# Performance work log

Hardware: AMD Instinct MI355X
Metric: run time of the kernel (lower is better)

## Reference

```python
import jax, jax.numpy as jnp
import numpy as np


def _average(x, w, W):
    """layers.Average forward: weighted mean over batch of Linear(x) (bias=False).
    x: [N, d_in], w: [N, 1], W: [d_out, d_in] -> [1, d_out]"""
    h = x @ W.T                                    # [N, d_out]
    return jnp.sum(h * w, axis=0, keepdims=True) / jnp.sum(w)


def setup_inputs() -> dict:
    key = jax.random.key(0)
    k1, k2, k3, k4 = jax.random.split(key, 4)
    N, n_in, n_middle = 1_000_000, 32, 128
    x = jax.random.normal(k1, (N, n_in), dtype=jnp.float32)
    w = jax.random.uniform(k2, (N, 1), dtype=jnp.float32)
    # Linear weights (Kaiming-ish scale), bias=False per __init__ default
    W_in = jax.random.normal(k3, (n_middle, n_in), dtype=jnp.float32) / np.float32(np.sqrt(n_in))
    W_out = jax.random.normal(k4, (n_in, n_middle), dtype=jnp.float32) / np.float32(np.sqrt(n_middle))
    return {"x": x, "w": w, "W_in": W_in, "W_out": W_out}


def reference(x, w, W_in, W_out):
    # x_ = activation(avg_in(x, w))
    h = jax.nn.relu(_average(x, w, W_in))          # [1, n_middle]
    # x_ = avg_out(x_, w); residual add (broadcast over batch)
    x_ = _average(h, w, W_out)                     # [1, n_in]
    return x + x_                                  # [N, n_in]
```

## Files before the change

### kernel.cpp

```cpp
#include <hip/hip_runtime.h>

#define BS 256
#define NB1 2048
#define NB3 2048

typedef float vfloat4 __attribute__((ext_vector_type(4)));

__global__ void __launch_bounds__(BS) reduce_kernel(
    const float* __restrict__ x, const float* __restrict__ w,
    float* __restrict__ colpart, float* __restrict__ wpart, long long total4) {
  const int tid = threadIdx.x;
  const long long stride2 = (long long)gridDim.x * (2 * BS);
  const vfloat4* x4 = (const vfloat4*)x;
  vfloat4 a0 = (vfloat4)(0.f);
  vfloat4 a1 = (vfloat4)(0.f);
  float w0 = 0.f, w1 = 0.f;
  long long c = (long long)blockIdx.x * (2 * BS) + tid;
  for (; c + BS < total4; c += stride2) {
    const float wi0 = w[(int)(c >> 3)];
    const float wi1 = w[(int)((c + BS) >> 3)];
    const vfloat4 v0 = x4[c];
    const vfloat4 v1 = x4[c + BS];
    a0 += wi0 * v0;
    a1 += wi1 * v1;
    w0 += wi0; w1 += wi1;
  }
  if (c < total4) {
    const float wi = w[(int)(c >> 3)];
    a0 += wi * x4[c];
    w0 += wi;
  }
  a0 += a1;
  w0 += w1;
  __shared__ vfloat4 sacc[BS];
  __shared__ float   sw[BS];
  sacc[tid] = a0;
  sw[tid] = w0;
  __syncthreads();
  for (int s = BS / 2; s >= 8; s >>= 1) {
    if (tid < s) {
      sacc[tid] += sacc[tid + s];
      sw[tid] += sw[tid + s];
    }
    __syncthreads();
  }
  if (tid < 8) {
    ((vfloat4*)(colpart + (long long)blockIdx.x * 32))[tid] = sacc[tid];
  }
  if (tid == 0) {
    wpart[blockIdx.x] = sw[0] + sw[1] + sw[2] + sw[3] +
                        sw[4] + sw[5] + sw[6] + sw[7];
  }
}

__global__ void __launch_bounds__(BS) middle_kernel(
    const float* __restrict__ colpart, const float* __restrict__ wpart,
    const float* __restrict__ W_in, const float* __restrict__ W_out,
    float* __restrict__ r_out, int nb) {
  const int tid = threadIdx.x;
  __shared__ vfloat4 sacc[BS];
  __shared__ float   swr[BS];
  __shared__ float   avg[32];
  __shared__ float   h[128];
  {
    const vfloat4* cp4 = (const vfloat4*)colpart;
    const int nchunk = nb * 8;
    vfloat4 acc = (vfloat4)(0.f);
    for (int cb = tid; cb < nchunk; cb += BS) acc += cp4[cb];
    sacc[tid] = acc;
  }
  {
    const vfloat4* wp4 = (const vfloat4*)wpart;
    const int nchunk = nb / 4;
    float s = 0.f;
    for (int cb = tid; cb < nchunk; cb += BS) {
      vfloat4 v = wp4[cb];
      s += v.x + v.y + v.z + v.w;
    }
    swr[tid] = s;
  }
  __syncthreads();
  for (int s = BS / 2; s >= 8; s >>= 1) {
    if (tid < s) {
      sacc[tid] += sacc[tid + s];
      swr[tid] += swr[tid + s];
    }
    __syncthreads();
  }
  if (tid == 0) {
    float wsum = (swr[0] + swr[1] + swr[2] + swr[3] +
                  swr[4] + swr[5] + swr[6] + swr[7]) * 0.125f;
    swr[0] = wsum;
  }
  __syncthreads();
  if (tid < 32) {
    const float* sflat = (const float*)sacc;
    avg[tid] = sflat[tid] / swr[0];
  }
  __syncthreads();
  if (tid < 128) {
    float a = 0.f;
    for (int k = 0; k < 32; ++k) a = fmaf(W_in[tid * 32 + k], avg[k], a);
    h[tid] = fmaxf(a, 0.f);
  }
  __syncthreads();
  if (tid < 32) {
    float r = 0.f;
    for (int k = 0; k < 128; ++k) r = fmaf(W_out[tid * 128 + k], h[k], r);
    r_out[tid] = r;
  }
}

__global__ void __launch_bounds__(BS) add_kernel(
    const float* __restrict__ x, const float* __restrict__ r,
    float* __restrict__ out, long long total4) {
  const int tid = threadIdx.x;
  const vfloat4 rr = ((const vfloat4*)r)[tid & 7];
  const long long stride2 = (long long)gridDim.x * (2 * BS);
  const vfloat4* x4 = (const vfloat4*)x;
  vfloat4* o4 = (vfloat4*)out;
  long long c = (long long)blockIdx.x * (2 * BS) + tid;
  for (; c + BS < total4; c += stride2) {
    vfloat4 v0 = x4[c] + rr;
    vfloat4 v1 = x4[c + BS] + rr;
    __builtin_nontemporal_store(v0, &o4[c]);
    __builtin_nontemporal_store(v1, &o4[c + BS]);
  }
  if (c < total4) {
    vfloat4 v = x4[c] + rr;
    __builtin_nontemporal_store(v, &o4[c]);
  }
}

extern "C" void kernel_launch(void* const* d_in, const int* in_sizes, int n_in,
                              void* d_out, int out_size, void* d_ws, size_t ws_size,
                              hipStream_t stream) {
  const float* x     = (const float*)d_in[0];
  const float* w     = (const float*)d_in[1];
  const float* W_in  = (const float*)d_in[2];
  const float* W_out = (const float*)d_in[3];
  float* out = (float*)d_out;

  const long long N = (long long)in_sizes[0] / 32;
  const long long total4 = N * 8;

  int nb = NB1;
  while (nb > 64 && (size_t)(nb * 33 + 32) * 4 > ws_size) nb >>= 1;
  float* colpart = (float*)d_ws;
  float* wpart   = colpart + (size_t)nb * 32;
  float* r       = wpart + nb;

  reduce_kernel<<<nb, BS, 0, stream>>>(x, w, colpart, wpart, total4);
  middle_kernel<<<1, BS, 0, stream>>>(colpart, wpart, W_in, W_out, r, nb);
  add_kernel<<<NB3, BS, 0, stream>>>(x, r, out, total4);
}
```

Baseline: 265.5 us.

## Fuse reduce, MLP and residual-add into one cooperative kernel with grid sync

Merges the three kernel launches into a single cooperative kernel. Each block does a partial weighted reduction, the grid syncs, then every block redundantly re-reduces the partials and computes the tiny MLP. Each block then adds the result to x over the same grid-stride range it reduced, so that slice of x may still be in cache. This removes two launch gaps and the extra round trip for r. In exchange every block repeats the middle computation, the grid barrier adds cost, and the grid drops to 1024 blocks, which may lower memory-level parallelism.

```diff
diff --git a/kernel.cpp b/kernel.cpp
--- a/kernel.cpp
+++ b/kernel.cpp
@@ -1,41 +1,47 @@
 #include <hip/hip_runtime.h>
+#include <hip/hip_cooperative_groups.h>
 
 #define BS 256
-#define NB1 2048
-#define NB3 2048
+#define NB 1024
 
 typedef float vfloat4 __attribute__((ext_vector_type(4)));
 
-__global__ void __launch_bounds__(BS) reduce_kernel(
+__global__ void __launch_bounds__(BS, 4) fused_kernel(
     const float* __restrict__ x, const float* __restrict__ w,
-    float* __restrict__ colpart, float* __restrict__ wpart, long long total4) {
+    const float* __restrict__ W_in, const float* __restrict__ W_out,
+    float* __restrict__ out, float* __restrict__ colpart,
+    float* __restrict__ wpart, long long total4) {
   const int tid = threadIdx.x;
   const long long stride2 = (long long)gridDim.x * (2 * BS);
+  const long long c0 = (long long)blockIdx.x * (2 * BS) + tid;
   const vfloat4* x4 = (const vfloat4*)x;
-  vfloat4 a0 = (vfloat4)(0.f);
-  vfloat4 a1 = (vfloat4)(0.f);
-  float w0 = 0.f, w1 = 0.f;
-  long long c = (long long)blockIdx.x * (2 * BS) + tid;
-  for (; c + BS < total4; c += stride2) {
-    const float wi0 = w[(int)(c >> 3)];
-    const float wi1 = w[(int)((c + BS) >> 3)];
-    const vfloat4 v0 = x4[c];
-    const vfloat4 v1 = x4[c + BS];
-    a0 += wi0 * v0;
-    a1 += wi1 * v1;
-    w0 += wi0; w1 += wi1;
-  }
-  if (c < total4) {
-    const float wi = w[(int)(c >> 3)];
-    a0 += wi * x4[c];
-    w0 += wi;
-  }
-  a0 += a1;
-  w0 += w1;
+
   __shared__ vfloat4 sacc[BS];
   __shared__ float   sw[BS];
-  sacc[tid] = a0;
-  sw[tid] = w0;
+  __shared__ float   avg[32];
+  __shared__ float   h[128];
+  __shared__ float   rsh[32];
+
+  {
+    vfloat4 a0 = (vfloat4)(0.f), a1 = (vfloat4)(0.f);
+    float w0 = 0.f, w1 = 0.f;
+    long long c = c0;
+    for (; c + BS < total4; c += stride2) {
+      const float wi0 = w[(int)(c >> 3)];
+      const float wi1 = w[(int)((c + BS) >> 3)];
+      a0 += wi0 * x4[c];
+      a1 += wi1 * x4[c + BS];
+      w0 += wi0; w1 += wi1;
+    }
+    if (c < total4) {
+      const float wi = w[(int)(c >> 3)];
+      a0 += wi * x4[c];
+      w0 += wi;
+    }
+    a0 += a1; w0 += w1;
+    sacc[tid] = a0;
+    sw[tid] = w0;
+  }
   __syncthreads();
   for (int s = BS / 2; s >= 8; s >>= 1) {
     if (tid < s) {
@@ -51,51 +57,39 @@
     wpart[blockIdx.x] = sw[0] + sw[1] + sw[2] + sw[3] +
                         sw[4] + sw[5] + sw[6] + sw[7];
   }
-}
+  __threadfence();
+  cooperative_groups::this_grid().sync();
+  __threadfence();
 
-__global__ void __launch_bounds__(BS) middle_kernel(
-    const float* __restrict__ colpart, const float* __restrict__ wpart,
-    const float* __restrict__ W_in, const float* __restrict__ W_out,
-    float* __restrict__ r_out, int nb) {
-  const int tid = threadIdx.x;
-  __shared__ vfloat4 sacc[BS];
-  __shared__ float   swr[BS];
-  __shared__ float   avg[32];
-  __shared__ float   h[128];
   {
     const vfloat4* cp4 = (const vfloat4*)colpart;
-    const int nchunk = nb * 8;
     vfloat4 acc = (vfloat4)(0.f);
-    for (int cb = tid; cb < nchunk; cb += BS) acc += cp4[cb];
+    for (int cb = tid; cb < NB * 8; cb += BS) acc += cp4[cb];
     sacc[tid] = acc;
-  }
-  {
     const vfloat4* wp4 = (const vfloat4*)wpart;
-    const int nchunk = nb / 4;
     float s = 0.f;
-    for (int cb = tid; cb < nchunk; cb += BS) {
+    for (int cb = tid; cb < NB / 4; cb += BS) {
       vfloat4 v = wp4[cb];
       s += v.x + v.y + v.z + v.w;
     }
-    swr[tid] = s;
+    sw[tid] = s;
   }
   __syncthreads();
   for (int s = BS / 2; s >= 8; s >>= 1) {
     if (tid < s) {
       sacc[tid] += sacc[tid + s];
-      swr[tid] += swr[tid + s];
+      sw[tid] += sw[tid + s];
     }
     __syncthreads();
   }
   if (tid == 0) {
-    float wsum = (swr[0] + swr[1] + swr[2] + swr[3] +
-                  swr[4] + swr[5] + swr[6] + swr[7]) * 0.125f;
-    swr[0] = wsum;
+    sw[0] = (sw[0] + sw[1] + sw[2] + sw[3] +
+             sw[4] + sw[5] + sw[6] + sw[7]) * 0.125f;
   }
   __syncthreads();
   if (tid < 32) {
     const float* sflat = (const float*)sacc;
-    avg[tid] = sflat[tid] / swr[0];
+    avg[tid] = sflat[tid] / sw[0];
   }
   __syncthreads();
   if (tid < 128) {
@@ -107,28 +101,24 @@
   if (tid < 32) {
     float r = 0.f;
     for (int k = 0; k < 128; ++k) r = fmaf(W_out[tid * 128 + k], h[k], r);
-    r_out[tid] = r;
+    rsh[tid] = r;
   }
-}
+  __syncthreads();
 
-__global__ void __launch_bounds__(BS) add_kernel(
-    const float* __restrict__ x, const float* __restrict__ r,
-    float* __restrict__ out, long long total4) {
-  const int tid = threadIdx.x;
-  const vfloat4 rr = ((const vfloat4*)r)[tid & 7];
-  const long long stride2 = (long long)gridDim.x * (2 * BS);
-  const vfloat4* x4 = (const vfloat4*)x;
-  vfloat4* o4 = (vfloat4*)out;
-  long long c = (long long)blockIdx.x * (2 * BS) + tid;
-  for (; c + BS < total4; c += stride2) {
-    vfloat4 v0 = x4[c] + rr;
-    vfloat4 v1 = x4[c + BS] + rr;
-    __builtin_nontemporal_store(v0, &o4[c]);
-    __builtin_nontemporal_store(v1, &o4[c + BS]);
-  }
-  if (c < total4) {
-    vfloat4 v = x4[c] + rr;
-    __builtin_nontemporal_store(v, &o4[c]);
+  {
+    const vfloat4 rr = ((const vfloat4*)rsh)[tid & 7];
+    vfloat4* o4 = (vfloat4*)out;
+    long long c = c0;
+    for (; c + BS < total4; c += stride2) {
+      vfloat4 v0 = x4[c] + rr;
+      vfloat4 v1 = x4[c + BS] + rr;
+      __builtin_nontemporal_store(v0, &o4[c]);
+      __builtin_nontemporal_store(v1, &o4[c + BS]);
+    }
+    if (c < total4) {
+      vfloat4 v = x4[c] + rr;
+      __builtin_nontemporal_store(v, &o4[c]);
+    }
   }
 }
 
@@ -142,15 +132,13 @@
   float* out = (float*)d_out;
 
   const long long N = (long long)in_sizes[0] / 32;
-  const long long total4 = N * 8;
+  long long total4 = N * 8;
 
-  int nb = NB1;
-  while (nb > 64 && (size_t)(nb * 33 + 32) * 4 > ws_size) nb >>= 1;
   float* colpart = (float*)d_ws;
-  float* wpart   = colpart + (size_t)nb * 32;
-  float* r       = wpart + nb;
+  float* wpart   = colpart + (size_t)NB * 32;
 
-  reduce_kernel<<<nb, BS, 0, stream>>>(x, w, colpart, wpart, total4);
-  middle_kernel<<<1, BS, 0, stream>>>(colpart, wpart, W_in, W_out, r, nb);
-  add_kernel<<<NB3, BS, 0, stream>>>(x, r, out, total4);
+  void* args[] = {(void*)&x, (void*)&w, (void*)&W_in, (void*)&W_out,
+                  (void*)&out, (void*)&colpart, (void*)&wpart, (void*)&total4};
+  hipLaunchCooperativeKernel((const void*)fused_kernel, dim3(NB), dim3(BS),
+                             args, 0, stream);
 }
```

After: 434.5 us. 63.7% more time.
